# Optimization experiments

Measured on AMD Instinct MI355X. Metric: run time of the kernel, lower is better.

Reference implementation:

```python
import jax, jax.numpy as jnp
import numpy as np

B, S, N, D = 2, 2048, 16, 64


def setup_inputs() -> dict:
    key = jax.random.key(0)
    kq, kk, kv = jax.random.split(key, 3)
    query = jax.random.normal(kq, (B, S, N, D), dtype=jnp.float32)
    key_t = jax.random.normal(kk, (B, S, N, D), dtype=jnp.float32)
    value = jax.random.normal(kv, (B, S, N, D), dtype=jnp.float32)
    mask = jnp.ones((B, 1, S, S), dtype=jnp.int32)
    return {"query": query, "key": key_t, "value": value, "mask": mask}


def reference(query, key, value, mask):
    d_k = query.shape[-1]
    # [b, n, q, k] attention scores
    scores = jnp.einsum('bqnd,bknd->bnqk', query, key) / jnp.sqrt(jnp.float32(d_k))
    scores = jnp.where(mask == 0, -jnp.inf, scores)
    # NOTE: faithful to the source, softmax is over dim=1 (the HEAD axis),
    # not the key axis. Dropout prob is 0.0 -> identity.
    attn_weights = jax.nn.softmax(scores, axis=1)
    out = jnp.einsum('bnqk,bknd->bnqd', attn_weights, value)
    return out
```

## Files before the change

kernel.cpp:

```cpp
#include <hip/hip_runtime.h>
#include <hip/hip_bf16.h>


#define B_ 2
#define S_ 2048
#define N_ 16
#define D_ 64
#define TQ 32
#define TK 32
#define NT 64

typedef __bf16 bf16x4 __attribute__((ext_vector_type(4)));
typedef __bf16 bf16x8 __attribute__((ext_vector_type(8)));
typedef float  f32x16 __attribute__((ext_vector_type(16)));
typedef unsigned int uint32x4 __attribute__((ext_vector_type(4)));

#define QSCALE 0.18033688011112042f

static __device__ __forceinline__ unsigned int cvt_pk_bf16(float a, float b) {
    unsigned int r;
    asm("v_cvt_pk_bf16_f32 %0, %1, %2" : "=v"(r) : "v"(a), "v"(b));
    return r;
}
static __device__ __forceinline__ void permlane_swap(unsigned int& a, unsigned int& b) {
    asm("v_permlane32_swap_b32 %0, %1" : "+v"(a), "+v"(b));
}

__global__ __launch_bounds__(256) void cvt_qk_pack_kernel(
    const float* __restrict__ Qf, const float* __restrict__ Kf,
    __bf16* __restrict__ QP, __bf16* __restrict__ KP)
{
    const int z = blockIdx.z;
    const float* src = (z < B_) ? Qf : Kf;
    __bf16*      dst = (z < B_) ? QP : KP;
    const float scale = (z < B_) ? QSCALE : 1.0f;
    const int b  = (z < B_) ? z : z - B_;
    const int n  = blockIdx.y;
    const int st = blockIdx.x;
    const int t  = threadIdx.x;
    const int ks   = t >> 6;
    const int lane = t & 63;
    const int lo   = lane & 31;
    const int hi   = lane >> 5;

    const float* p = &src[(((size_t)b * S_ + st * 32 + lo) * N_ + n) * D_ + ks * 16 + hi * 8];
    const float4 a0 = *(const float4*)p;
    const float4 a1 = *(const float4*)(p + 4);
    bf16x8 o;
    o[0] = (__bf16)(a0.x * scale); o[1] = (__bf16)(a0.y * scale);
    o[2] = (__bf16)(a0.z * scale); o[3] = (__bf16)(a0.w * scale);
    o[4] = (__bf16)(a1.x * scale); o[5] = (__bf16)(a1.y * scale);
    o[6] = (__bf16)(a1.z * scale); o[7] = (__bf16)(a1.w * scale);
    *(bf16x8*)&dst[(((size_t)b * N_ + n) * NT + st) * 2048 + (size_t)t * 8] = o;
}

__global__ __launch_bounds__(256) void cvt_v_pack_kernel(
    const float* __restrict__ V, __bf16* __restrict__ VP)
{
    __shared__ __bf16 tile[64][68];
    const int s0 = blockIdx.x * 64;
    const int n  = blockIdx.y;
    const int b  = blockIdx.z;
    const int t  = threadIdx.x;

    {
        const int d4 = (t & 15) * 4;
        const int sr = t >> 4;
        #pragma unroll
        for (int r = 0; r < 4; ++r) {
            const int s = sr + r * 16;
            const float4 v = *(const float4*)&V[(((size_t)b * S_ + s0 + s) * N_ + n) * D_ + d4];
            tile[s][d4 + 0] = (__bf16)v.x;
            tile[s][d4 + 1] = (__bf16)v.y;
            tile[s][d4 + 2] = (__bf16)v.z;
            tile[s][d4 + 3] = (__bf16)v.w;
        }
    }
    __syncthreads();
    {
        const int kstep = t >> 7;
        const int dt    = (t >> 6) & 1;
        const int lane  = t & 63;
        const int lo    = lane & 31;
        const int hi    = lane >> 5;
        #pragma unroll
        for (int kt_sub = 0; kt_sub < 2; ++kt_sub) {
            bf16x8 o;
            #pragma unroll
            for (int j = 0; j < 8; ++j)
                o[j] = tile[kt_sub * 32 + kstep * 16 + hi * 8 + j][dt * 32 + lo];
            const size_t kt = (size_t)(blockIdx.x * 2 + kt_sub);
            *(bf16x8*)&VP[(((size_t)b * N_ + n) * NT + kt) * 2048 + (size_t)t * 8] = o;
        }
    }
}

__global__ __launch_bounds__(256, 2) void pass1_z_kernel(
    const __bf16* __restrict__ QP, const __bf16* __restrict__ KP,
    const int* __restrict__ M, __bf16* __restrict__ Zrb)
{
    const int tid  = threadIdx.x;
    const int wv   = tid >> 6;
    const int lane = tid & 63;
    const int lo   = lane & 31;
    const int hi   = lane >> 5;

    const int ktA = (blockIdx.x * 4 + wv) * 2;
    const int qt0 = blockIdx.y * 2;
    const int b   = blockIdx.z;
    const int k0A = ktA * TK;
    const int q0  = qt0 * TQ;

    const __bf16* Qp = QP + ((size_t)b * N_ * NT + qt0) * 2048 + (size_t)lane * 8;
    const __bf16* Kp = KP + ((size_t)b * N_ * NT + ktA) * 2048 + (size_t)lane * 8;

    f32x16 zAA = {}, zAB = {}, zBA = {}, zBB = {};
    for (int h = 0; h < N_; ++h) {
        const __bf16* Qh = Qp + (size_t)h * NT * 2048;
        const __bf16* Kh = Kp + (size_t)h * NT * 2048;
        bf16x8 q0f[4], q1f[4], ka[4], kb[4];
        #pragma unroll
        for (int ks = 0; ks < 4; ++ks) {
            q0f[ks] = *(const bf16x8*)(Qh + ks * 512);
            q1f[ks] = *(const bf16x8*)(Qh + 2048 + ks * 512);
            ka[ks]  = *(const bf16x8*)(Kh + ks * 512);
            kb[ks]  = *(const bf16x8*)(Kh + 2048 + ks * 512);
        }
        f32x16 s;
        s = (f32x16){};
        #pragma unroll
        for (int ks = 0; ks < 4; ++ks) s = __builtin_amdgcn_mfma_f32_32x32x16_bf16(ka[ks], q0f[ks], s, 0, 0, 0);
        #pragma unroll
        for (int r = 0; r < 16; ++r) zAA[r] += __builtin_amdgcn_exp2f(s[r]);
        s = (f32x16){};
        #pragma unroll
        for (int ks = 0; ks < 4; ++ks) s = __builtin_amdgcn_mfma_f32_32x32x16_bf16(ka[ks], q1f[ks], s, 0, 0, 0);
        #pragma unroll
        for (int r = 0; r < 16; ++r) zAB[r] += __builtin_amdgcn_exp2f(s[r]);
        s = (f32x16){};
        #pragma unroll
        for (int ks = 0; ks < 4; ++ks) s = __builtin_amdgcn_mfma_f32_32x32x16_bf16(kb[ks], q0f[ks], s, 0, 0, 0);
        #pragma unroll
        for (int r = 0; r < 16; ++r) zBA[r] += __builtin_amdgcn_exp2f(s[r]);
        s = (f32x16){};
        #pragma unroll
        for (int ks = 0; ks < 4; ++ks) s = __builtin_amdgcn_mfma_f32_32x32x16_bf16(kb[ks], q1f[ks], s, 0, 0, 0);
        #pragma unroll
        for (int r = 0; r < 16; ++r) zBB[r] += __builtin_amdgcn_exp2f(s[r]);
    }

    const size_t mb = (size_t)b * S_ * S_;
    int ok = 1;
    #pragma unroll
    for (int r = 0; r < 16; ++r) {
        const int4 mm = *(const int4*)&M[mb + (size_t)(q0 + 4 * r + (lane >> 4)) * S_
                                         + k0A + (lane & 15) * 4];
        ok &= (mm.x != 0) & (mm.y != 0) & (mm.z != 0) & (mm.w != 0);
    }

    float vAA[16], vAB[16], vBA[16], vBB[16];
    #pragma unroll
    for (int r = 0; r < 16; ++r) {
        vAA[r] = __builtin_amdgcn_rcpf(zAA[r]);
        vAB[r] = __builtin_amdgcn_rcpf(zAB[r]);
        vBA[r] = __builtin_amdgcn_rcpf(zBA[r]);
        vBB[r] = __builtin_amdgcn_rcpf(zBB[r]);
    }

    if (!__all(ok)) {
        #pragma unroll
        for (int r = 0; r < 16; ++r) {
            const int kap = (r & 3) + 8 * (r >> 2) + 4 * hi;
            const size_t rowA = mb + (size_t)(q0 + lo) * S_;
            const size_t rowB = mb + (size_t)(q0 + 32 + lo) * S_;
            if (M[rowA + k0A + kap] == 0)      vAA[r] = __builtin_nanf("");
            if (M[rowB + k0A + kap] == 0)      vAB[r] = __builtin_nanf("");
            if (M[rowA + k0A + 32 + kap] == 0) vBA[r] = __builtin_nanf("");
            if (M[rowB + k0A + 32 + kap] == 0) vBB[r] = __builtin_nanf("");
        }
    }

    auto store_tile = [&](const float (&v)[16], int kt_, int qt_) {
        __bf16* Zt = Zrb + (((size_t)b * NT + kt_) * NT + qt_) * 1024 + (size_t)lane * 8;
        #pragma unroll
        for (int g = 0; g < 2; ++g) {
            uint32x4 u;
            #pragma unroll
            for (int i = 0; i < 4; ++i)
                u[i] = cvt_pk_bf16(v[g * 8 + 2 * i], v[g * 8 + 2 * i + 1]);
            *(bf16x8*)(Zt + g * 512) = __builtin_bit_cast(bf16x8, u);
        }
    };
    store_tile(vAA, ktA,     qt0);
    store_tile(vAB, ktA,     qt0 + 1);
    store_tile(vBA, ktA + 1, qt0);
    store_tile(vBB, ktA + 1, qt0 + 1);
}

__global__ __launch_bounds__(256, 4) void pass2_av_kernel(
    const __bf16* __restrict__ QP, const __bf16* __restrict__ KP,
    const __bf16* __restrict__ VP, const __bf16* __restrict__ Zrb,
    float* __restrict__ O)
{
    __shared__ __align__(16) float obuf[4][16 * D_];

    const int tid  = threadIdx.x;
    const int wv   = tid >> 6;
    const int lane = tid & 63;
    const int lo   = lane & 31;
    const int hi   = lane >> 5;

    const int n  = blockIdx.x;
    const int qt = blockIdx.y;
    const int b  = blockIdx.z;
    const int q0 = qt * TQ;

    const __bf16* Qh = QP + (((size_t)b * N_ + n) * NT + qt) * 2048 + (size_t)lane * 8;
    const __bf16* Kh = KP + (((size_t)b * N_ + n) * NT) * 2048 + (size_t)lane * 8;
    const __bf16* Vh = VP + (((size_t)b * N_ + n) * NT) * 2048 + (size_t)lane * 8;
    const __bf16* Zb = Zrb + (size_t)b * NT * NT * 1024 + (size_t)lane * 8;

    bf16x8 qf[4];
    #pragma unroll
    for (int ks = 0; ks < 4; ++ks)
        qf[ks] = *(const bf16x8*)(Qh + ks * 512);

    f32x16 o0 = {};
    f32x16 o1 = {};

    #pragma unroll 2
    for (int t = 0; t < 16; ++t) {
        const int kt = wv * 16 + t;
        const __bf16* Kt = Kh + (size_t)kt * 2048;
        const __bf16* Vt = Vh + (size_t)kt * 2048;
        const __bf16* Zt = Zb + ((size_t)kt * NT + qt) * 1024;

        const bf16x8 za = *(const bf16x8*)(Zt);
        const bf16x8 zb = *(const bf16x8*)(Zt + 512);

        bf16x8 kf[4];
        #pragma unroll
        for (int ks = 0; ks < 4; ++ks) kf[ks] = *(const bf16x8*)(Kt + ks * 512);
        bf16x8 vf[2][2];
        #pragma unroll
        for (int kstep = 0; kstep < 2; ++kstep)
            #pragma unroll
            for (int dt = 0; dt < 2; ++dt)
                vf[kstep][dt] = *(const bf16x8*)(Vt + (kstep * 2 + dt) * 512);

        f32x16 s = {};
        #pragma unroll
        for (int ks = 0; ks < 4; ++ks)
            s = __builtin_amdgcn_mfma_f32_32x32x16_bf16(kf[ks], qf[ks], s, 0, 0, 0);

        float w[16];
        #pragma unroll
        for (int r = 0; r < 8; ++r)  w[r] = __builtin_amdgcn_exp2f(s[r]) * (float)za[r];
        #pragma unroll
        for (int r = 8; r < 16; ++r) w[r] = __builtin_amdgcn_exp2f(s[r]) * (float)zb[r - 8];

        #pragma unroll
        for (int kstep = 0; kstep < 2; ++kstep) {
            const int e = kstep * 8;
            unsigned int d0 = cvt_pk_bf16(w[e + 0], w[e + 1]);
            unsigned int d1 = cvt_pk_bf16(w[e + 2], w[e + 3]);
            unsigned int d2 = cvt_pk_bf16(w[e + 4], w[e + 5]);
            unsigned int d3 = cvt_pk_bf16(w[e + 6], w[e + 7]);
            permlane_swap(d0, d2);
            permlane_swap(d1, d3);
            uint32x4 u; u[0] = d0; u[1] = d1; u[2] = d2; u[3] = d3;
            const bf16x8 pa = __builtin_bit_cast(bf16x8, u);
            o0 = __builtin_amdgcn_mfma_f32_32x32x16_bf16(pa, vf[kstep][0], o0, 0, 0, 0);
            o1 = __builtin_amdgcn_mfma_f32_32x32x16_bf16(pa, vf[kstep][1], o1, 0, 0, 0);
        }
    }

    #pragma unroll
    for (int half = 0; half < 2; ++half) {
        if (half) __syncthreads();
        #pragma unroll
        for (int r8 = 0; r8 < 8; ++r8) {
            const int r  = half * 8 + r8;
            const int lr = (r8 & 3) + 8 * (r8 >> 2) + 4 * hi;
            obuf[wv][lr * D_ + lo]      = o0[r];
            obuf[wv][lr * D_ + 32 + lo] = o1[r];
        }
        __syncthreads();
        const int e0 = tid * 4;
        float a0 = 0.f, a1 = 0.f, a2 = 0.f, a3 = 0.f;
        #pragma unroll
        for (int w = 0; w < 4; ++w) {
            const float4 x = *(const float4*)&obuf[w][e0];
            a0 += x.x; a1 += x.y; a2 += x.z; a3 += x.w;
        }
        const int q = half * 16 + (e0 >> 6);
        const int d = e0 & 63;
        *(float4*)&O[(((size_t)b * N_ + n) * S_ + q0 + q) * (size_t)D_ + d]
            = make_float4(a0, a1, a2, a3);
    }
}

__global__ __launch_bounds__(1024) void sdpa_headsm_kernel(
    const float* __restrict__ Q, const float* __restrict__ K,
    const float* __restrict__ V, const int* __restrict__ M,
    float* __restrict__ O)
{
    __shared__ __align__(16) __bf16 pbuf[N_][TQ][40];

    const int tid  = threadIdx.x;
    const int n    = tid >> 6;
    const int lane = tid & 63;
    const int lo   = lane & 31;
    const int hi   = lane >> 5;

    const int q0 = blockIdx.x * TQ;
    const int b  = blockIdx.y;
    const int kz = blockIdx.z;
    const int FITERS = S_ / TK / 4;

    bf16x8 qf[4];
    {
        const float* qrow = Q + (((size_t)b * S_ + (size_t)(q0 + lo)) * N_ + n) * D_;
        #pragma unroll
        for (int ks = 0; ks < 4; ++ks) {
            const float* p = qrow + ks * 16 + hi * 8;
            float4 a0 = *(const float4*)(p);
            float4 a1 = *(const float4*)(p + 4);
            bf16x8 f;
            f[0] = (__bf16)a0.x; f[1] = (__bf16)a0.y;
            f[2] = (__bf16)a0.z; f[3] = (__bf16)a0.w;
            f[4] = (__bf16)a1.x; f[5] = (__bf16)a1.y;
            f[6] = (__bf16)a1.z; f[7] = (__bf16)a1.w;
            qf[ks] = f;
        }
    }

    f32x16 o0 = {};
    f32x16 o1 = {};

    for (int it = 0; it < FITERS; ++it) {
        const int k0 = (kz * FITERS + it) * TK;

        f32x16 s = {};
        #pragma unroll
        for (int ks = 0; ks < 4; ++ks) {
            const float* krow = K + (((size_t)b * S_ + (size_t)(k0 + lo)) * N_ + n) * D_
                                  + ks * 16 + hi * 8;
            float4 a0 = *(const float4*)(krow);
            float4 a1 = *(const float4*)(krow + 4);
            bf16x8 f;
            f[0] = (__bf16)a0.x; f[1] = (__bf16)a0.y;
            f[2] = (__bf16)a0.z; f[3] = (__bf16)a0.w;
            f[4] = (__bf16)a1.x; f[5] = (__bf16)a1.y;
            f[6] = (__bf16)a1.z; f[7] = (__bf16)a1.w;
            s = __builtin_amdgcn_mfma_f32_32x32x16_bf16(qf[ks], f, s, 0, 0, 0);
        }

        bf16x8 vf[2][2];
        #pragma unroll
        for (int kstep = 0; kstep < 2; ++kstep) {
            #pragma unroll
            for (int dt = 0; dt < 2; ++dt) {
                bf16x8 f;
                #pragma unroll
                for (int j = 0; j < 8; ++j) {
                    const int key = k0 + kstep * 16 + hi * 8 + j;
                    f[j] = (__bf16)V[(((size_t)b * S_ + key) * N_ + n) * D_ + dt * 32 + lo];
                }
                vf[kstep][dt] = f;
            }
        }

        #pragma unroll
        for (int r = 0; r < 16; ++r) {
            const int row = (r & 3) + 8 * (r >> 2) + 4 * hi;
            pbuf[n][row][lo] = (__bf16)__builtin_amdgcn_exp2f(s[r] * QSCALE);
        }

        __syncthreads();

        {
            const int tq = tid >> 5;
            const int tk = tid & 31;
            const int m = M[(size_t)b * S_ * S_ + (size_t)(q0 + tq) * S_ + (k0 + tk)];
            float pv[16];
            float sum = 0.f;
            #pragma unroll
            for (int j = 0; j < 16; ++j) { pv[j] = (float)pbuf[j][tq][tk]; sum += pv[j]; }
            const float rd = m ? (1.0f / sum) : __builtin_nanf("");
            #pragma unroll
            for (int j = 0; j < 16; ++j) pbuf[j][tq][tk] = (__bf16)(pv[j] * rd);
        }

        __syncthreads();

        #pragma unroll
        for (int kstep = 0; kstep < 2; ++kstep) {
            bf16x8 wf = *(const bf16x8*)&pbuf[n][lo][kstep * 16 + hi * 8];
            o0 = __builtin_amdgcn_mfma_f32_32x32x16_bf16(wf, vf[kstep][0], o0, 0, 0, 0);
            o1 = __builtin_amdgcn_mfma_f32_32x32x16_bf16(wf, vf[kstep][1], o1, 0, 0, 0);
        }

        __syncthreads();
    }

    #pragma unroll
    for (int r = 0; r < 16; ++r) {
        const int row = (r & 3) + 8 * (r >> 2) + 4 * hi;
        const size_t base = (((size_t)b * N_ + n) * S_ + (q0 + row)) * (size_t)D_;
        atomicAdd(&O[base + lo],      o0[r]);
        atomicAdd(&O[base + 32 + lo], o1[r]);
    }
}

extern "C" void kernel_launch(void* const* d_in, const int* in_sizes, int n_in,
                              void* d_out, int out_size, void* d_ws, size_t ws_size,
                              hipStream_t stream) {
    const float* Q = (const float*)d_in[0];
    const float* K = (const float*)d_in[1];
    const float* V = (const float*)d_in[2];
    const int*   M = (const int*)d_in[3];
    float* O = (float*)d_out;

    const size_t per  = (size_t)B_ * N_ * NT * 2048;
    const size_t zcnt = (size_t)B_ * NT * NT * 1024;
    const size_t need = (3 * per + zcnt) * sizeof(__bf16);

    if (ws_size >= need) {
        __bf16* QP = (__bf16*)d_ws;
        __bf16* KP = QP + per;
        __bf16* VP = KP + per;
        __bf16* Zrb = VP + per;
        cvt_qk_pack_kernel<<<dim3(NT, N_, B_ * 2), dim3(256), 0, stream>>>(Q, K, QP, KP);
        cvt_v_pack_kernel<<<dim3(S_ / 64, N_, B_), dim3(256), 0, stream>>>(V, VP);
        pass1_z_kernel<<<dim3(NT / 8, NT / 2, B_), dim3(256), 0, stream>>>(QP, KP, M, Zrb);
        pass2_av_kernel<<<dim3(N_, NT, B_), dim3(256), 0, stream>>>(QP, KP, VP, Zrb, O);
    } else {
        hipMemsetAsync(d_out, 0, (size_t)out_size * sizeof(float), stream);
        sdpa_headsm_kernel<<<dim3(S_ / TQ, B_, 4), dim3(1024), 0, stream>>>(Q, K, V, M, O);
    }
}
```

Measured before the change: 216.1 us.

## Store head-softmax reciprocal normalizers in fp32 and reorder pass2 grid

The per-(q,k) reciprocal softmax denominators Z go into the workspace as fp32 instead of bf16, using float4 stores and loads laid out per lane. The pass-2 grid is also swapped so q-tiles vary fastest and heads sit on the y axis, which changes which blocks share Z tiles in cache. This doubles Z traffic and workspace size, and drops the bf16 conversion cost and rounding error. The grid reorder is meant to improve L2 reuse of Z across concurrently running blocks.

```diff
diff --git a/kernel.cpp b/kernel.cpp
--- a/kernel.cpp
+++ b/kernel.cpp
@@ -97,7 +97,7 @@
 
 __global__ __launch_bounds__(256, 2) void pass1_z_kernel(
     const __bf16* __restrict__ QP, const __bf16* __restrict__ KP,
-    const int* __restrict__ M, __bf16* __restrict__ Zrb)
+    const int* __restrict__ M, float* __restrict__ Zr)
 {
     const int tid  = threadIdx.x;
     const int wv   = tid >> 6;
@@ -181,15 +181,10 @@
     }
 
     auto store_tile = [&](const float (&v)[16], int kt_, int qt_) {
-        __bf16* Zt = Zrb + (((size_t)b * NT + kt_) * NT + qt_) * 1024 + (size_t)lane * 8;
-        #pragma unroll
-        for (int g = 0; g < 2; ++g) {
-            uint32x4 u;
-            #pragma unroll
-            for (int i = 0; i < 4; ++i)
-                u[i] = cvt_pk_bf16(v[g * 8 + 2 * i], v[g * 8 + 2 * i + 1]);
-            *(bf16x8*)(Zt + g * 512) = __builtin_bit_cast(bf16x8, u);
-        }
+        float* Zt = Zr + (((size_t)b * NT + kt_) * NT + qt_) * 1024 + (size_t)lane * 4;
+        #pragma unroll
+        for (int c = 0; c < 4; ++c)
+            *(float4*)(Zt + c * 256) = make_float4(v[4*c], v[4*c+1], v[4*c+2], v[4*c+3]);
     };
     store_tile(vAA, ktA,     qt0);
     store_tile(vAB, ktA,     qt0 + 1);
@@ -199,7 +194,7 @@
 
 __global__ __launch_bounds__(256, 4) void pass2_av_kernel(
     const __bf16* __restrict__ QP, const __bf16* __restrict__ KP,
-    const __bf16* __restrict__ VP, const __bf16* __restrict__ Zrb,
+    const __bf16* __restrict__ VP, const float* __restrict__ Zr,
     float* __restrict__ O)
 {
     __shared__ __align__(16) float obuf[4][16 * D_];
@@ -210,15 +205,15 @@
     const int lo   = lane & 31;
     const int hi   = lane >> 5;
 
-    const int n  = blockIdx.x;
-    const int qt = blockIdx.y;
+    const int qt = blockIdx.x;
+    const int n  = blockIdx.y;
     const int b  = blockIdx.z;
     const int q0 = qt * TQ;
 
     const __bf16* Qh = QP + (((size_t)b * N_ + n) * NT + qt) * 2048 + (size_t)lane * 8;
     const __bf16* Kh = KP + (((size_t)b * N_ + n) * NT) * 2048 + (size_t)lane * 8;
     const __bf16* Vh = VP + (((size_t)b * N_ + n) * NT) * 2048 + (size_t)lane * 8;
-    const __bf16* Zb = Zrb + (size_t)b * NT * NT * 1024 + (size_t)lane * 8;
+    const float*  Zb = Zr + (size_t)b * NT * NT * 1024 + (size_t)lane * 4;
 
     bf16x8 qf[4];
     #pragma unroll
@@ -233,10 +228,14 @@
         const int kt = wv * 16 + t;
         const __bf16* Kt = Kh + (size_t)kt * 2048;
         const __bf16* Vt = Vh + (size_t)kt * 2048;
-        const __bf16* Zt = Zb + ((size_t)kt * NT + qt) * 1024;
-
-        const bf16x8 za = *(const bf16x8*)(Zt);
-        const bf16x8 zb = *(const bf16x8*)(Zt + 512);
+        const float*  Zt = Zb + ((size_t)kt * NT + qt) * 1024;
+
+        float4 z0 = *(const float4*)(Zt);
+        float4 z1 = *(const float4*)(Zt + 256);
+        float4 z2 = *(const float4*)(Zt + 512);
+        float4 z3 = *(const float4*)(Zt + 768);
+        float zr[16] = { z0.x, z0.y, z0.z, z0.w,  z1.x, z1.y, z1.z, z1.w,
+                         z2.x, z2.y, z2.z, z2.w,  z3.x, z3.y, z3.z, z3.w };
 
         bf16x8 kf[4];
         #pragma unroll
@@ -255,9 +254,7 @@
 
         float w[16];
         #pragma unroll
-        for (int r = 0; r < 8; ++r)  w[r] = __builtin_amdgcn_exp2f(s[r]) * (float)za[r];
-        #pragma unroll
-        for (int r = 8; r < 16; ++r) w[r] = __builtin_amdgcn_exp2f(s[r]) * (float)zb[r - 8];
+        for (int r = 0; r < 16; ++r) w[r] = __builtin_amdgcn_exp2f(s[r]) * zr[r];
 
         #pragma unroll
         for (int kstep = 0; kstep < 2; ++kstep) {
@@ -424,17 +421,17 @@
 
     const size_t per  = (size_t)B_ * N_ * NT * 2048;
     const size_t zcnt = (size_t)B_ * NT * NT * 1024;
-    const size_t need = (3 * per + zcnt) * sizeof(__bf16);
+    const size_t need = 3 * per * sizeof(__bf16) + zcnt * sizeof(float);
 
     if (ws_size >= need) {
         __bf16* QP = (__bf16*)d_ws;
         __bf16* KP = QP + per;
         __bf16* VP = KP + per;
-        __bf16* Zrb = VP + per;
+        float*  Zr = (float*)(VP + per);
         cvt_qk_pack_kernel<<<dim3(NT, N_, B_ * 2), dim3(256), 0, stream>>>(Q, K, QP, KP);
         cvt_v_pack_kernel<<<dim3(S_ / 64, N_, B_), dim3(256), 0, stream>>>(V, VP);
-        pass1_z_kernel<<<dim3(NT / 8, NT / 2, B_), dim3(256), 0, stream>>>(QP, KP, M, Zrb);
-        pass2_av_kernel<<<dim3(N_, NT, B_), dim3(256), 0, stream>>>(QP, KP, VP, Zrb, O);
+        pass1_z_kernel<<<dim3(NT / 8, NT / 2, B_), dim3(256), 0, stream>>>(QP, KP, M, Zr);
+        pass2_av_kernel<<<dim3(NT, N_, B_), dim3(256), 0, stream>>>(QP, KP, VP, Zr, O);
     } else {
         hipMemsetAsync(d_out, 0, (size_t)out_size * sizeof(float), stream);
         sdpa_headsm_kernel<<<dim3(S_ / TQ, B_, 4), dim3(1024), 0, stream>>>(Q, K, V, M, O);
```

Measured after the change: 212.7 us. About the same (-1.6%).
